# Performance work log

Measured on AMD Instinct MI355X. Metric: run time of the kernel, lower is better.

Reference implementation:

```python
import jax, jax.numpy as jnp
import numpy as np

N_NODES = 100000


def _add_self_loops(edge_index, n):
    loop = jnp.arange(n, dtype=edge_index.dtype)
    src = jnp.concatenate([edge_index[0], loop])
    dst = jnp.concatenate([edge_index[1], loop])
    return src, dst


def gcn_conv(x, edge_index, W, b):
    # x: [N, Fin], edge_index: [2, E]; PyG GCNConv with add_self_loops + symmetric norm
    n = x.shape[0]
    src, dst = _add_self_loops(edge_index, n)
    # degree of augmented graph (counting incoming edges at dst, weight 1)
    deg = jax.ops.segment_sum(jnp.ones_like(dst, dtype=x.dtype), dst, num_segments=n)
    dinv = jnp.where(deg > 0, jax.lax.rsqrt(deg), 0.0)
    norm = dinv[src] * dinv[dst]                      # [E+N]
    h = x @ W                                         # [N, Fout] (transform first: Fout small)
    msg = h[src] * norm[:, None]                      # gather + scale
    out = jax.ops.segment_sum(msg, dst, num_segments=n)  # scatter-add
    return out + b


def setup_inputs() -> dict:
    key = jax.random.key(0)
    k1, k2, k3, k4, k5, k6 = jax.random.split(key, 6)
    F_in, H, C = 512, 16, 40
    x = jax.random.normal(k1, (N_NODES, F_in), dtype=jnp.float32)
    edge_index = jax.random.randint(k2, (2, 3200000), 0, N_NODES, dtype=jnp.int64)
    s1 = 1.0 / np.sqrt(F_in)
    s2 = 1.0 / np.sqrt(H)
    W1 = jax.random.uniform(k3, (F_in, H), jnp.float32, -s1, s1)
    b1 = jax.random.uniform(k4, (H,), jnp.float32, -s1, s1)
    W2 = jax.random.uniform(k5, (H, C), jnp.float32, -s2, s2)
    b2 = jax.random.uniform(k6, (C,), jnp.float32, -s2, s2)
    return {"x": x, "edge_index": edge_index, "W1": W1, "b1": b1, "W2": W2, "b2": b2}


def reference(x, edge_index, W1, b1, W2, b2):
    h = gcn_conv(x, edge_index, W1, b1)
    h = jax.nn.relu(h)
    # F.dropout(training=False) -> identity at inference
    h = gcn_conv(h, edge_index, W2, b2)
    return jax.nn.log_softmax(h, axis=1)
```

## Files before the change

kernel.cpp:

```cpp
#include <hip/hip_runtime.h>

#define N_NODES 100000
#define N_EDGES 3200000
#define FIN 512
#define FH 16
#define FC 40
#define NB_N ((N_NODES + 255) / 256)
#define NBKT 391
#define NBLK_P 256
#define CHUNK (N_EDGES / NBLK_P)

typedef int   ivec4 __attribute__((ext_vector_type(4)));
typedef float fvec4 __attribute__((ext_vector_type(4)));


__global__ __launch_bounds__(256) void kA1(const int* __restrict__ dst,
                                           int* __restrict__ H) {
  __shared__ int h[NBKT];
  int t = threadIdx.x;
  for (int i = t; i < NBKT; i += 256) h[i] = 0;
  __syncthreads();
  const ivec4* d4 = (const ivec4*)(dst + blockIdx.x * CHUNK);
  for (int i = t; i < CHUNK / 4; i += 256) {
    ivec4 v = __builtin_nontemporal_load(d4 + i);
    atomicAdd(&h[v.x >> 8], 1);
    atomicAdd(&h[v.y >> 8], 1);
    atomicAdd(&h[v.z >> 8], 1);
    atomicAdd(&h[v.w >> 8], 1);
  }
  __syncthreads();
  for (int i = t; i < NBKT; i += 256) H[blockIdx.x * NBKT + i] = h[i];
}


__global__ __launch_bounds__(256) void kA2(const int* __restrict__ H,
                                           int* __restrict__ P,
                                           int* __restrict__ T) {
  __shared__ int s[256];
  int t = threadIdx.x, b = blockIdx.x;
  int v = H[t * NBKT + b];
  s[t] = v;
  __syncthreads();
  for (int d = 1; d < 256; d <<= 1) {
    int x = (t >= d) ? s[t - d] : 0;
    __syncthreads();
    s[t] += x;
    __syncthreads();
  }
  P[t * NBKT + b] = s[t] - v;
  if (t == 255) T[b] = s[t];
}


__global__ __launch_bounds__(512) void kA3s(const int* __restrict__ T,
                                            int* __restrict__ Base,
                                            int* __restrict__ off) {
  __shared__ int s[512];
  int t = threadIdx.x;
  int v = (t < NBKT) ? T[t] : 0;
  s[t] = v;
  __syncthreads();
  for (int d = 1; d < 512; d <<= 1) {
    int x = (t >= d) ? s[t - d] : 0;
    __syncthreads();
    s[t] += x;
    __syncthreads();
  }
  if (t < NBKT) Base[t] = s[t] - v;
  if (t == 0) off[N_NODES] = N_EDGES;
}


__global__ __launch_bounds__(256) void kA3(const int* __restrict__ ei,
                                           const int* __restrict__ Base,
                                           const int* __restrict__ P,
                                           int* __restrict__ stage) {
  __shared__ int cur[NBKT];
  int t = threadIdx.x, blk = blockIdx.x;
  for (int i = t; i < NBKT; i += 256) cur[i] = Base[i] + P[blk * NBKT + i];
  __syncthreads();
  int base = blk * CHUNK;
  const ivec4* s4 = (const ivec4*)(ei + base);
  const ivec4* d4 = (const ivec4*)(ei + N_EDGES + base);
  for (int i = t; i < CHUNK / 4; i += 256) {
    ivec4 sv = __builtin_nontemporal_load(s4 + i);
    ivec4 dv = __builtin_nontemporal_load(d4 + i);
    int slot;
    slot = atomicAdd(&cur[dv.x >> 8], 1);
    __builtin_nontemporal_store(sv.x | ((dv.x & 255) << 17), stage + slot);
    slot = atomicAdd(&cur[dv.y >> 8], 1);
    __builtin_nontemporal_store(sv.y | ((dv.y & 255) << 17), stage + slot);
    slot = atomicAdd(&cur[dv.z >> 8], 1);
    __builtin_nontemporal_store(sv.z | ((dv.z & 255) << 17), stage + slot);
    slot = atomicAdd(&cur[dv.w >> 8], 1);
    __builtin_nontemporal_store(sv.w | ((dv.w & 255) << 17), stage + slot);
  }
}


__global__ __launch_bounds__(256) void kB(const int* __restrict__ stage,
                                          const int* __restrict__ Base,
                                          const int* __restrict__ T,
                                          int* __restrict__ off,
                                          int* __restrict__ csr,
                                          float* __restrict__ dinv) {
  __shared__ int hist[256], cursor[256], sc[256];
  int t = threadIdx.x, b = blockIdx.x;
  int base = Base[b], cnt = T[b];
  hist[t] = 0;
  __syncthreads();
  for (int i = t; i < cnt; i += 256) atomicAdd(&hist[stage[base + i] >> 17], 1);
  __syncthreads();
  int c = hist[t];
  sc[t] = c;
  __syncthreads();
  for (int d = 1; d < 256; d <<= 1) {
    int x = (t >= d) ? sc[t - d] : 0;
    __syncthreads();
    sc[t] += x;
    __syncthreads();
  }
  int excl = sc[t] - c;
  int node = b * 256 + t;
  if (node < N_NODES) {
    off[node] = base + excl;
    dinv[node] = rsqrtf((float)(c + 1));
  }
  cursor[t] = excl;
  __syncthreads();
  for (int i = t; i < cnt; i += 256) {
    int pk = stage[base + i];
    int slot = atomicAdd(&cursor[pk >> 17], 1);
    csr[base + slot] = pk & 0x1FFFF;
  }
}


__global__ __launch_bounds__(256) void k_gemm1(const float* __restrict__ x,
                                               const float* __restrict__ W1,
                                               const float* __restrict__ dinv,
                                               float* __restrict__ p1) {
  __shared__ float xs[256 * 36];
  const int t = threadIdx.x;
  const int row0 = blockIdx.x * 256;
  const int row = row0 + t;
  float acc[FH];
#pragma unroll
  for (int c = 0; c < FH; c++) acc[c] = 0.0f;

  const fvec4 zero4 = {0.f, 0.f, 0.f, 0.f};
  fvec4 ld[8];
#pragma unroll
  for (int i = 0; i < 8; i++) {
    int idx = t + 256 * i;
    int r = idx >> 3, c4 = idx & 7;
    int gr = row0 + r;
    ld[i] = (gr < N_NODES)
                ? __builtin_nontemporal_load(
                      (const fvec4*)(x + (size_t)gr * FIN + 0 + c4 * 4))
                : zero4;
  }

  for (int kc = 0; kc < FIN; kc += 32) {
    __syncthreads();
#pragma unroll
    for (int i = 0; i < 8; i++) {
      int idx = t + 256 * i;
      int r = idx >> 3, c4 = idx & 7;
      *(fvec4*)(&xs[r * 36 + c4 * 4]) = ld[i];
    }
    __syncthreads();
    if (kc + 32 < FIN) {
#pragma unroll
      for (int i = 0; i < 8; i++) {
        int idx = t + 256 * i;
        int r = idx >> 3, c4 = idx & 7;
        int gr = row0 + r;
        ld[i] = (gr < N_NODES)
                    ? __builtin_nontemporal_load(
                          (const fvec4*)(x + (size_t)gr * FIN + (kc + 32) + c4 * 4))
                    : zero4;
      }
    }
    float4 xr[8];
#pragma unroll
    for (int q = 0; q < 8; q++) xr[q] = *(const float4*)(&xs[t * 36 + q * 4]);
    const float4* w4 = (const float4*)(W1 + (size_t)kc * FH);
#pragma unroll
    for (int k = 0; k < 32; k++) {
      float xv = ((const float*)xr)[k];
      float4 wa = w4[k * 4 + 0], wb = w4[k * 4 + 1];
      float4 wc = w4[k * 4 + 2], wd = w4[k * 4 + 3];
      acc[0] = fmaf(xv, wa.x, acc[0]);   acc[1] = fmaf(xv, wa.y, acc[1]);
      acc[2] = fmaf(xv, wa.z, acc[2]);   acc[3] = fmaf(xv, wa.w, acc[3]);
      acc[4] = fmaf(xv, wb.x, acc[4]);   acc[5] = fmaf(xv, wb.y, acc[5]);
      acc[6] = fmaf(xv, wb.z, acc[6]);   acc[7] = fmaf(xv, wb.w, acc[7]);
      acc[8] = fmaf(xv, wc.x, acc[8]);   acc[9] = fmaf(xv, wc.y, acc[9]);
      acc[10] = fmaf(xv, wc.z, acc[10]); acc[11] = fmaf(xv, wc.w, acc[11]);
      acc[12] = fmaf(xv, wd.x, acc[12]); acc[13] = fmaf(xv, wd.y, acc[13]);
      acc[14] = fmaf(xv, wd.z, acc[14]); acc[15] = fmaf(xv, wd.w, acc[15]);
    }
  }

  if (row < N_NODES) {
    float dv = dinv[row];
#pragma unroll
    for (int c = 0; c < FH; c++) acc[c] *= dv;
#pragma unroll
    for (int q = 0; q < 4; q++)
      *(float4*)(p1 + (size_t)row * FH + q * 4) = ((const float4*)acc)[q];
  }
}


__global__ __launch_bounds__(256) void k_gather1(const int* __restrict__ off,
                                                 const int* __restrict__ csr,
                                                 const float* __restrict__ p1,
                                                 const float* __restrict__ dinv,
                                                 const float* __restrict__ b1,
                                                 float* __restrict__ q) {
  int lane = threadIdx.x & 63;
  int node = blockIdx.x * 4 + (threadIdx.x >> 6);
  int start = off[node];
  int end = off[node + 1];
  int slot = lane >> 2, comp = lane & 3;
  float4 acc = make_float4(0.f, 0.f, 0.f, 0.f);
  if (slot == 0)
    acc = *(const float4*)(p1 + (size_t)node * FH + comp * 4);
  for (int base = start; base < end; base += 32) {
    int e0 = base + slot, e1 = e0 + 16;
    int s0 = (e0 < end) ? __builtin_nontemporal_load(csr + e0) : -1;
    int s1 = (e1 < end) ? __builtin_nontemporal_load(csr + e1) : -1;
    if (s0 >= 0) {
      float4 v = *(const float4*)(p1 + (size_t)s0 * FH + comp * 4);
      acc.x += v.x; acc.y += v.y; acc.z += v.z; acc.w += v.w;
    }
    if (s1 >= 0) {
      float4 v = *(const float4*)(p1 + (size_t)s1 * FH + comp * 4);
      acc.x += v.x; acc.y += v.y; acc.z += v.z; acc.w += v.w;
    }
  }
#pragma unroll
  for (int m = 4; m <= 32; m <<= 1) {
    acc.x += __shfl_xor(acc.x, m);
    acc.y += __shfl_xor(acc.y, m);
    acc.z += __shfl_xor(acc.z, m);
    acc.w += __shfl_xor(acc.w, m);
  }
  float dv = dinv[node];
  if (lane < 4) {
    float4 bb = *(const float4*)(b1 + lane * 4);
    float4 r;
    r.x = fmaxf(fmaf(acc.x, dv, bb.x), 0.f) * dv;
    r.y = fmaxf(fmaf(acc.y, dv, bb.y), 0.f) * dv;
    r.z = fmaxf(fmaf(acc.z, dv, bb.z), 0.f) * dv;
    r.w = fmaxf(fmaf(acc.w, dv, bb.w), 0.f) * dv;
    *(float4*)(q + (size_t)node * FH + lane * 4) = r;
  }
}


__global__ __launch_bounds__(256) void k_gather2(const int* __restrict__ off,
                                                 const int* __restrict__ csr,
                                                 const float* __restrict__ q,
                                                 const float* __restrict__ dinv,
                                                 const float* __restrict__ W2,
                                                 const float* __restrict__ b2,
                                                 float* __restrict__ out) {
  int lane = threadIdx.x & 63;
  int node = blockIdx.x * 4 + (threadIdx.x >> 6);
  int start = off[node];
  int end = off[node + 1];
  int slot = lane >> 2, comp = lane & 3;
  float4 acc = make_float4(0.f, 0.f, 0.f, 0.f);
  if (slot == 0)
    acc = *(const float4*)(q + (size_t)node * FH + comp * 4);
  for (int base = start; base < end; base += 32) {
    int e0 = base + slot, e1 = e0 + 16;
    int s0 = (e0 < end) ? __builtin_nontemporal_load(csr + e0) : -1;
    int s1 = (e1 < end) ? __builtin_nontemporal_load(csr + e1) : -1;
    if (s0 >= 0) {
      float4 v = *(const float4*)(q + (size_t)s0 * FH + comp * 4);
      acc.x += v.x; acc.y += v.y; acc.z += v.z; acc.w += v.w;
    }
    if (s1 >= 0) {
      float4 v = *(const float4*)(q + (size_t)s1 * FH + comp * 4);
      acc.x += v.x; acc.y += v.y; acc.z += v.z; acc.w += v.w;
    }
  }
#pragma unroll
  for (int m = 4; m <= 32; m <<= 1) {
    acc.x += __shfl_xor(acc.x, m);
    acc.y += __shfl_xor(acc.y, m);
    acc.z += __shfl_xor(acc.z, m);
    acc.w += __shfl_xor(acc.w, m);
  }
  float dv = dinv[node];
  acc.x *= dv; acc.y *= dv; acc.z *= dv; acc.w *= dv;
  float t16[16];
  t16[comp * 4 + 0] = acc.x; t16[comp * 4 + 1] = acc.y;
  t16[comp * 4 + 2] = acc.z; t16[comp * 4 + 3] = acc.w;
#pragma unroll
  for (int m = 1; m <= 3; m++) {
    int oc = comp ^ m;
    t16[oc * 4 + 0] = __shfl_xor(acc.x, m);
    t16[oc * 4 + 1] = __shfl_xor(acc.y, m);
    t16[oc * 4 + 2] = __shfl_xor(acc.z, m);
    t16[oc * 4 + 3] = __shfl_xor(acc.w, m);
  }
  float z = -1e30f;
  if (lane < FC) {
    z = b2[lane];
#pragma unroll
    for (int k = 0; k < FH; k++) z = fmaf(t16[k], W2[k * FC + lane], z);
  }
  float mx = z;
#pragma unroll
  for (int d = 1; d < 64; d <<= 1) mx = fmaxf(mx, __shfl_xor(mx, d));
  float ex = (lane < FC) ? __expf(z - mx) : 0.f;
#pragma unroll
  for (int d = 1; d < 64; d <<= 1) ex += __shfl_xor(ex, d);
  float l = __logf(ex) + mx;
  if (lane < FC) out[(size_t)node * FC + lane] = z - l;
}


extern "C" void kernel_launch(void* const* d_in, const int* in_sizes, int n_in,
                              void* d_out, int out_size, void* d_ws, size_t ws_size,
                              hipStream_t stream) {
  const float* x  = (const float*)d_in[0];
  const int*   ei = (const int*)d_in[1];
  const float* W1 = (const float*)d_in[2];
  const float* b1 = (const float*)d_in[3];
  const float* W2 = (const float*)d_in[4];
  const float* b2 = (const float*)d_in[5];
  float* out = (float*)d_out;

  int* wsi  = (int*)d_ws;
  int* H    = wsi;
  int* P    = H + 100096;
  int* T    = P + 100096;
  int* Base = T + 512;
  int* off  = Base + 512;
  int* csr  = off + 100352;
  int* stage = csr + 3200000;
  float* dinv = (float*)(stage + 3200000);
  float* p1 = (float*)stage;
  float* q  = p1 + 1600000;

  kA1 <<<NBLK_P, 256, 0, stream>>>(ei + N_EDGES, H);
  kA2 <<<NBKT,   256, 0, stream>>>(H, P, T);
  kA3s<<<1,      512, 0, stream>>>(T, Base, off);
  kA3 <<<NBLK_P, 256, 0, stream>>>(ei, Base, P, stage);
  kB  <<<NBKT,   256, 0, stream>>>(stage, Base, T, off, csr, dinv);
  k_gemm1  <<<NB_N, 256, 0, stream>>>(x, W1, dinv, p1);
  k_gather1<<<N_NODES / 4, 256, 0, stream>>>(off, csr, p1, dinv, b1, q);
  k_gather2<<<N_NODES / 4, 256, 0, stream>>>(off, csr, q, dinv, W2, b2, out);
}
```

Before: 593.2 us.

## Replace two-pass bucket sort CSR build with global-atomic counting sort

Replaces the LDS-bucketed two-level radix-style CSR construction (block histograms, staging array, per-bucket local sort) with a direct global-atomic degree count, a three-kernel prefix scan, and a placement pass that uses global atomic cursors per node. This removes the staging buffer write/read and the second sort pass, but relies on 3.2M global atomics twice, with scattered CSR writes and nondeterministic in-row edge order. It also drops the register prefetch double-buffering in the first GEMM, replacing it with plain loads inside the loop.

```diff
diff --git a/kernel.cpp b/kernel.cpp
--- a/kernel.cpp
+++ b/kernel.cpp
@@ -6,39 +6,38 @@
 #define FH 16
 #define FC 40
 #define NB_N ((N_NODES + 255) / 256)
-#define NBKT 391
-#define NBLK_P 256
-#define CHUNK (N_EDGES / NBLK_P)
-
-typedef int   ivec4 __attribute__((ext_vector_type(4)));
-typedef float fvec4 __attribute__((ext_vector_type(4)));
-
-
-__global__ __launch_bounds__(256) void kA1(const int* __restrict__ dst,
-                                           int* __restrict__ H) {
-  __shared__ int h[NBKT];
-  int t = threadIdx.x;
-  for (int i = t; i < NBKT; i += 256) h[i] = 0;
-  __syncthreads();
-  const ivec4* d4 = (const ivec4*)(dst + blockIdx.x * CHUNK);
-  for (int i = t; i < CHUNK / 4; i += 256) {
+
+typedef int ivec4 __attribute__((ext_vector_type(4)));
+
+
+__global__ __launch_bounds__(256) void kZero(int* __restrict__ deg) {
+  int i = blockIdx.x * 256 + threadIdx.x;
+  if (i < 100352) deg[i] = 0;
+}
+
+
+__global__ __launch_bounds__(256) void kDeg(const int* __restrict__ dst,
+                                            int* __restrict__ deg) {
+  const ivec4* d4 = (const ivec4*)dst;
+  for (int i = blockIdx.x * 256 + threadIdx.x; i < N_EDGES / 4;
+       i += gridDim.x * 256) {
     ivec4 v = __builtin_nontemporal_load(d4 + i);
-    atomicAdd(&h[v.x >> 8], 1);
-    atomicAdd(&h[v.y >> 8], 1);
-    atomicAdd(&h[v.z >> 8], 1);
-    atomicAdd(&h[v.w >> 8], 1);
-  }
-  __syncthreads();
-  for (int i = t; i < NBKT; i += 256) H[blockIdx.x * NBKT + i] = h[i];
-}
-
-
-__global__ __launch_bounds__(256) void kA2(const int* __restrict__ H,
-                                           int* __restrict__ P,
-                                           int* __restrict__ T) {
+    atomicAdd(&deg[v.x], 1);
+    atomicAdd(&deg[v.y], 1);
+    atomicAdd(&deg[v.z], 1);
+    atomicAdd(&deg[v.w], 1);
+  }
+}
+
+
+__global__ __launch_bounds__(256) void kScan1(const int* __restrict__ deg,
+                                              int* __restrict__ off,
+                                              int* __restrict__ T,
+                                              float* __restrict__ dinv) {
   __shared__ int s[256];
   int t = threadIdx.x, b = blockIdx.x;
-  int v = H[t * NBKT + b];
+  int node = b * 256 + t;
+  int v = (node < N_NODES) ? deg[node] : 0;
   s[t] = v;
   __syncthreads();
   for (int d = 1; d < 256; d <<= 1) {
@@ -47,17 +46,20 @@
     s[t] += x;
     __syncthreads();
   }
-  P[t * NBKT + b] = s[t] - v;
+  if (node < N_NODES) {
+    off[node] = s[t] - v;
+    dinv[node] = rsqrtf((float)(v + 1));
+  }
   if (t == 255) T[b] = s[t];
 }
 
 
-__global__ __launch_bounds__(512) void kA3s(const int* __restrict__ T,
-                                            int* __restrict__ Base,
-                                            int* __restrict__ off) {
+__global__ __launch_bounds__(512) void kScan2(const int* __restrict__ T,
+                                              int* __restrict__ Base,
+                                              int* __restrict__ off) {
   __shared__ int s[512];
   int t = threadIdx.x;
-  int v = (t < NBKT) ? T[t] : 0;
+  int v = (t < NB_N) ? T[t] : 0;
   s[t] = v;
   __syncthreads();
   for (int d = 1; d < 512; d <<= 1) {
@@ -66,72 +68,42 @@
     s[t] += x;
     __syncthreads();
   }
-  if (t < NBKT) Base[t] = s[t] - v;
+  if (t < NB_N) Base[t] = s[t] - v;
   if (t == 0) off[N_NODES] = N_EDGES;
 }
 
 
-__global__ __launch_bounds__(256) void kA3(const int* __restrict__ ei,
-                                           const int* __restrict__ Base,
-                                           const int* __restrict__ P,
-                                           int* __restrict__ stage) {
-  __shared__ int cur[NBKT];
-  int t = threadIdx.x, blk = blockIdx.x;
-  for (int i = t; i < NBKT; i += 256) cur[i] = Base[i] + P[blk * NBKT + i];
-  __syncthreads();
-  int base = blk * CHUNK;
-  const ivec4* s4 = (const ivec4*)(ei + base);
-  const ivec4* d4 = (const ivec4*)(ei + N_EDGES + base);
-  for (int i = t; i < CHUNK / 4; i += 256) {
+__global__ __launch_bounds__(256) void kScan3(int* __restrict__ off,
+                                              const int* __restrict__ Base,
+                                              int* __restrict__ cursor) {
+  int t = threadIdx.x, b = blockIdx.x;
+  int node = b * 256 + t;
+  if (node < N_NODES) {
+    int o = off[node] + Base[b];
+    off[node] = o;
+    cursor[node] = o;
+  }
+}
+
+
+__global__ __launch_bounds__(256) void kPlace(const int* __restrict__ ei,
+                                              int* __restrict__ cursor,
+                                              int* __restrict__ csr) {
+  const ivec4* s4 = (const ivec4*)ei;
+  const ivec4* d4 = (const ivec4*)(ei + N_EDGES);
+  for (int i = blockIdx.x * 256 + threadIdx.x; i < N_EDGES / 4;
+       i += gridDim.x * 256) {
     ivec4 sv = __builtin_nontemporal_load(s4 + i);
     ivec4 dv = __builtin_nontemporal_load(d4 + i);
     int slot;
-    slot = atomicAdd(&cur[dv.x >> 8], 1);
-    __builtin_nontemporal_store(sv.x | ((dv.x & 255) << 17), stage + slot);
-    slot = atomicAdd(&cur[dv.y >> 8], 1);
-    __builtin_nontemporal_store(sv.y | ((dv.y & 255) << 17), stage + slot);
-    slot = atomicAdd(&cur[dv.z >> 8], 1);
-    __builtin_nontemporal_store(sv.z | ((dv.z & 255) << 17), stage + slot);
-    slot = atomicAdd(&cur[dv.w >> 8], 1);
-    __builtin_nontemporal_store(sv.w | ((dv.w & 255) << 17), stage + slot);
-  }
-}
-
-
-__global__ __launch_bounds__(256) void kB(const int* __restrict__ stage,
-                                          const int* __restrict__ Base,
-                                          const int* __restrict__ T,
-                                          int* __restrict__ off,
-                                          int* __restrict__ csr,
-                                          float* __restrict__ dinv) {
-  __shared__ int hist[256], cursor[256], sc[256];
-  int t = threadIdx.x, b = blockIdx.x;
-  int base = Base[b], cnt = T[b];
-  hist[t] = 0;
-  __syncthreads();
-  for (int i = t; i < cnt; i += 256) atomicAdd(&hist[stage[base + i] >> 17], 1);
-  __syncthreads();
-  int c = hist[t];
-  sc[t] = c;
-  __syncthreads();
-  for (int d = 1; d < 256; d <<= 1) {
-    int x = (t >= d) ? sc[t - d] : 0;
-    __syncthreads();
-    sc[t] += x;
-    __syncthreads();
-  }
-  int excl = sc[t] - c;
-  int node = b * 256 + t;
-  if (node < N_NODES) {
-    off[node] = base + excl;
-    dinv[node] = rsqrtf((float)(c + 1));
-  }
-  cursor[t] = excl;
-  __syncthreads();
-  for (int i = t; i < cnt; i += 256) {
-    int pk = stage[base + i];
-    int slot = atomicAdd(&cursor[pk >> 17], 1);
-    csr[base + slot] = pk & 0x1FFFF;
+    slot = atomicAdd(&cursor[dv.x], 1);
+    __builtin_nontemporal_store(sv.x, csr + slot);
+    slot = atomicAdd(&cursor[dv.y], 1);
+    __builtin_nontemporal_store(sv.y, csr + slot);
+    slot = atomicAdd(&cursor[dv.z], 1);
+    __builtin_nontemporal_store(sv.z, csr + slot);
+    slot = atomicAdd(&cursor[dv.w], 1);
+    __builtin_nontemporal_store(sv.w, csr + slot);
   }
 }
 
@@ -148,40 +120,25 @@
 #pragma unroll
   for (int c = 0; c < FH; c++) acc[c] = 0.0f;
 
-  const fvec4 zero4 = {0.f, 0.f, 0.f, 0.f};
-  fvec4 ld[8];
-#pragma unroll
-  for (int i = 0; i < 8; i++) {
-    int idx = t + 256 * i;
-    int r = idx >> 3, c4 = idx & 7;
-    int gr = row0 + r;
-    ld[i] = (gr < N_NODES)
-                ? __builtin_nontemporal_load(
-                      (const fvec4*)(x + (size_t)gr * FIN + 0 + c4 * 4))
-                : zero4;
-  }
-
   for (int kc = 0; kc < FIN; kc += 32) {
-    __syncthreads();
+    float4 ld[8];
 #pragma unroll
     for (int i = 0; i < 8; i++) {
       int idx = t + 256 * i;
       int r = idx >> 3, c4 = idx & 7;
-      *(fvec4*)(&xs[r * 36 + c4 * 4]) = ld[i];
-    }
-    __syncthreads();
-    if (kc + 32 < FIN) {
-#pragma unroll
-      for (int i = 0; i < 8; i++) {
-        int idx = t + 256 * i;
-        int r = idx >> 3, c4 = idx & 7;
-        int gr = row0 + r;
-        ld[i] = (gr < N_NODES)
-                    ? __builtin_nontemporal_load(
-                          (const fvec4*)(x + (size_t)gr * FIN + (kc + 32) + c4 * 4))
-                    : zero4;
-      }
-    }
+      int gr = row0 + r;
+      ld[i] = (gr < N_NODES)
+                  ? *(const float4*)(x + (size_t)gr * FIN + kc + c4 * 4)
+                  : make_float4(0.f, 0.f, 0.f, 0.f);
+    }
+    __syncthreads();
+#pragma unroll
+    for (int i = 0; i < 8; i++) {
+      int idx = t + 256 * i;
+      int r = idx >> 3, c4 = idx & 7;
+      *(float4*)(&xs[r * 36 + c4 * 4]) = ld[i];
+    }
+    __syncthreads();
     float4 xr[8];
 #pragma unroll
     for (int q = 0; q < 8; q++) xr[q] = *(const float4*)(&xs[t * 36 + q * 4]);
@@ -336,23 +293,23 @@
   const float* b2 = (const float*)d_in[5];
   float* out = (float*)d_out;
 
-  int* wsi  = (int*)d_ws;
-  int* H    = wsi;
-  int* P    = H + 100096;
-  int* T    = P + 100096;
-  int* Base = T + 512;
-  int* off  = Base + 512;
-  int* csr  = off + 100352;
-  int* stage = csr + 3200000;
-  float* dinv = (float*)(stage + 3200000);
-  float* p1 = (float*)stage;
-  float* q  = p1 + 1600000;
-
-  kA1 <<<NBLK_P, 256, 0, stream>>>(ei + N_EDGES, H);
-  kA2 <<<NBKT,   256, 0, stream>>>(H, P, T);
-  kA3s<<<1,      512, 0, stream>>>(T, Base, off);
-  kA3 <<<NBLK_P, 256, 0, stream>>>(ei, Base, P, stage);
-  kB  <<<NBKT,   256, 0, stream>>>(stage, Base, T, off, csr, dinv);
+  int* wsi    = (int*)d_ws;
+  int* deg    = wsi;
+  int* off    = deg + 100352;
+  int* cursor = off + 100352;
+  int* T      = cursor + 100352;
+  int* Base   = T + 512;
+  int* csr    = Base + 512;
+  float* dinv = (float*)(csr + 3200000);
+  float* p1   = dinv + 100352;
+  float* q    = p1 + 1600000;
+
+  kZero  <<<392,  256, 0, stream>>>(deg);
+  kDeg   <<<2048, 256, 0, stream>>>(ei + N_EDGES, deg);
+  kScan1 <<<NB_N, 256, 0, stream>>>(deg, off, T, dinv);
+  kScan2 <<<1,    512, 0, stream>>>(T, Base, off);
+  kScan3 <<<NB_N, 256, 0, stream>>>(off, Base, cursor);
+  kPlace <<<2048, 256, 0, stream>>>(ei, cursor, csr);
   k_gemm1  <<<NB_N, 256, 0, stream>>>(x, W1, dinv, p1);
   k_gather1<<<N_NODES / 4, 256, 0, stream>>>(off, csr, p1, dinv, b1, q);
   k_gather2<<<N_NODES / 4, 256, 0, stream>>>(off, csr, q, dinv, W2, b2, out);
```

Result: slower. 890.6 us (+50.1%).
